# Kernel tuning notes

Hardware: AMD Instinct MI355X
Metric: run time of the kernel (lower is better)

The kernel has to match this reference:

```python
import jax, jax.numpy as jnp
import numpy as np

INNER_LR = 0.01        # inner-loop fast-weight learning rate
ADAPTER_SCALE = 1.0    # adapter_scale from __init__
INIT_STD = 0.001       # init_std for phi_0 fast-weight initialization
VOCAB = 32000


def setup_inputs() -> dict:
    key = jax.random.key(0)
    k1, k2, k3, k4, k5 = jax.random.split(key, 5)
    B, S, H, R, V = 2, 2048, 1024, 16, VOCAB
    hidden_states = jax.random.normal(k1, (B, S, H), dtype=jnp.float32)
    input_ids = jax.random.randint(k2, (B, S), 0, V)
    # phi_0 learned fast-weight initialization (init_std-scaled, per TTTMetaAdapter)
    fast_a = jax.random.normal(k3, (H, R), dtype=jnp.float32) * INIT_STD
    fast_b = jax.random.normal(k4, (R, H), dtype=jnp.float32) * INIT_STD
    lm_head = jax.random.normal(k5, (H, V), dtype=jnp.float32) * 0.02
    return {"hidden_states": hidden_states, "input_ids": input_ids,
            "fast_a": fast_a, "fast_b": fast_b, "lm_head": lm_head}


def _next_token_loss(logits, input_ids):
    # ttt_next_token_loss_from_logits: CE(logits[:, :-1], input_ids[:, 1:])
    logp = jax.nn.log_softmax(logits[:, :-1, :], axis=-1)       # [B, S-1, V]
    tgt = input_ids[:, 1:]                                       # [B, S-1]
    nll = -jnp.take_along_axis(logp, tgt[..., None], axis=-1)[..., 0]
    return nll.mean()


def _apply(hidden_states, a, b):
    # TTTState.apply: h + (h @ fast_a @ fast_b) * scale
    return hidden_states + ((hidden_states @ a) @ b) * ADAPTER_SCALE


def reference(hidden_states, input_ids, fast_a, fast_b, lm_head):
    # Inner objective: next-token CE of adapted hidden states through lm_head.
    def inner_loss(a, b):
        adapted = _apply(hidden_states, a, b)                    # [B, S, H]
        logits = adapted @ lm_head                               # [B, S, V]
        return _next_token_loss(logits, input_ids)

    loss, (ga, gb) = jax.value_and_grad(inner_loss, argnums=(0, 1))(fast_a, fast_b)
    grad_norm = jnp.sqrt(jnp.sum(ga * ga) + jnp.sum(gb * gb))
    # One differentiable TTT inner gradient step on the fast weights.
    new_a = fast_a - INNER_LR * ga
    new_b = fast_b - INNER_LR * gb
    out = _apply(hidden_states, new_a, new_b)                    # adapted output
    return out, new_a, new_b, loss, grad_norm
```

## Files before the change

kernel.cpp:

```cpp
#include <hip/hip_runtime.h>
#include <hip/hip_bf16.h>


#define ROWS 4096
#define Hdim 1024
#define Rdim 16
#define Vdim 32000
#define NVALID 4094.0f
#define LRATE 0.01f
#define RB 32
#define VT 512

typedef __attribute__((ext_vector_type(8))) short bf16x8;
typedef __attribute__((ext_vector_type(4))) float f32x4;

static __device__ __forceinline__ float bf2f(short u) {
  union { float f; unsigned int i; } w; w.i = ((unsigned int)(unsigned short)u) << 16; return w.f;
}
static __device__ __forceinline__ short f2bf(float f) {
  union { float f; unsigned int i; } w; w.f = f;
  unsigned int lsb = (w.i >> 16) & 1u;
  w.i += 0x7fffu + lsb;
  return (short)(w.i >> 16);
}
static __device__ __forceinline__ f32x4 mfma16(bf16x8 a, bf16x8 b, f32x4 c) {
  return __builtin_amdgcn_mfma_f32_16x16x32_bf16(a, b, c, 0, 0, 0);
}

#define OFF_BP2   ((size_t)0)
#define OFF_BP1   ((size_t)65536000)
#define OFF_ADP   ((size_t)131072000)
#define OFF_DA    ((size_t)139460608)
#define OFF_U     ((size_t)156237824)
#define OFF_DU    ((size_t)156499968)
#define OFF_Z     ((size_t)157024256)
#define OFF_GA    ((size_t)157089792)
#define OFF_GB    ((size_t)157155328)
#define OFF_LOSS  ((size_t)157220864)

#define OUT_A    ((size_t)4194304)
#define OUT_B    ((size_t)4210688)
#define OUT_LOSS ((size_t)4227072)
#define OUT_GN   ((size_t)4227073)

__global__ void k_pack(const float* __restrict__ in, short* __restrict__ Bp1,
                       short* __restrict__ Bp2) {
  __shared__ short tile[32][258];
  int v0 = blockIdx.x * 256, k0 = blockIdx.y * 32;
  int tid = threadIdx.x;
#pragma unroll
  for (int r = 0; r < 32; ++r)
    tile[r][tid] = f2bf(in[(size_t)(k0 + r) * Vdim + v0 + tid]);
  __syncthreads();
  int lane = tid & 63, l15 = lane & 15, q = (lane >> 4) & 3, g = tid >> 6;
#pragma unroll
  for (int it = 0; it < 4; ++it) {
    int vbl = it * 4 + g;
    bf16x8 frag;
#pragma unroll
    for (int j = 0; j < 8; ++j) frag[j] = tile[q * 8 + j][vbl * 16 + l15];
    *(bf16x8*)(Bp1 + ((size_t)(v0 / 16 + vbl) * 32 + k0 / 32) * 512 + lane * 8) = frag;
  }
#pragma unroll
  for (int it = 0; it < 4; ++it) {
    int idx = it * 4 + g;
    int hbl = idx >> 3, vkbl = idx & 7;
    bf16x8 frag;
#pragma unroll
    for (int j = 0; j < 8; ++j) frag[j] = tile[hbl * 16 + l15][vkbl * 32 + q * 8 + j];
    *(bf16x8*)(Bp2 + ((size_t)(k0 / 16 + hbl) * 1000 + v0 / 32 + vkbl) * 512 + lane * 8) = frag;
  }
}

__global__ void k_prep_ua(const float* __restrict__ hs, const float* __restrict__ fa,
                          const float* __restrict__ fb, float* __restrict__ u,
                          short* __restrict__ adp) {
  __shared__ float wred[4][16];
  __shared__ float ubc[16];
  int row = blockIdx.x, tid = threadIdx.x, lane = tid & 63, w = tid >> 6;
  const float* hrow = hs + (size_t)row * Hdim;
  float4 hv = *(const float4*)(hrow + tid * 4);
  float ur[16];
  const float* fap = fa + (size_t)tid * 4 * Rdim;
#pragma unroll
  for (int r = 0; r < 16; ++r)
    ur[r] = hv.x * fap[r] + hv.y * fap[16 + r] + hv.z * fap[32 + r] + hv.w * fap[48 + r];
#pragma unroll
  for (int r = 0; r < 16; ++r)
#pragma unroll
    for (int off = 32; off; off >>= 1) ur[r] += __shfl_xor(ur[r], off);
  if (lane == 0) {
#pragma unroll
    for (int r = 0; r < 16; ++r) wred[w][r] = ur[r];
  }
  __syncthreads();
  if (tid < 16) {
    float s = wred[0][tid] + wred[1][tid] + wred[2][tid] + wred[3][tid];
    ubc[tid] = s;
    u[row * Rdim + tid] = s;
  }
  __syncthreads();
  float a0 = hv.x, a1 = hv.y, a2 = hv.z, a3 = hv.w;
#pragma unroll
  for (int r = 0; r < 16; ++r) {
    float uv = ubc[r];
    float4 bv = *(const float4*)(fb + r * Hdim + tid * 4);
    a0 += uv * bv.x; a1 += uv * bv.y; a2 += uv * bv.z; a3 += uv * bv.w;
  }
  short4 o; o.x = f2bf(a0); o.y = f2bf(a1); o.z = f2bf(a2); o.w = f2bf(a3);
  *(short4*)(adp + (size_t)row * Hdim + tid * 4) = o;
}

__launch_bounds__(1024, 4)
__global__ void k_fused(const short* __restrict__ adp, const short* __restrict__ Bp1,
                        const short* __restrict__ Bp2, short* __restrict__ dApart,
                        float* __restrict__ zpart) {
  __shared__ __align__(16) short lA[RB * 1024];
  __shared__ __align__(16) short lP[2][RB * VT];
  __shared__ float zred[RB * 16];
  int tid = threadIdx.x, lane = tid & 63, w = tid >> 6;
  int q = lane >> 4, l15 = lane & 15;
  int L = blockIdx.x;
  int sp = (L >> 2) & 1;
  int rg = (L & 3) | ((L >> 3) << 2);
  int row0 = rg * RB;
  int v0beg = sp ? 15872 : 0;
  int v0end = sp ? 32000 : 15872;
  int nt = sp ? 32 : 31;

#pragma unroll
  for (int i = 0; i < 4; ++i) {
    int idx = tid + i * 1024;
    int r = idx >> 7, c8 = (idx & 127) * 8;
    bf16x8 vv = *(const bf16x8*)(adp + (size_t)(row0 + r) * Hdim + c8);
    *(bf16x8*)((char*)lA + r * 2048 + ((c8 * 2) ^ ((r & 7) << 4))) = vv;
  }
  if (tid < RB * 16) zred[tid] = 0.f;

  float zacc[8];
  f32x4 acc[2][4];
#pragma unroll
  for (int j = 0; j < 8; ++j) zacc[j] = 0.f;
#pragma unroll
  for (int rf = 0; rf < 2; ++rf)
#pragma unroll
    for (int cf = 0; cf < 4; ++cf)
#pragma unroll
      for (int i = 0; i < 4; ++i) acc[rf][cf][i] = 0.f;

  __syncthreads();

  for (int t = 0; t < nt; ++t) {
    int v0 = v0beg + t * VT;
    int rem = v0end - v0; if (rem > VT) rem = VT;
    char* lPc = (char*)lP[t & 1];
    f32x4 lacc[2][2];
#pragma unroll
    for (int rf = 0; rf < 2; ++rf)
#pragma unroll
      for (int cf = 0; cf < 2; ++cf)
#pragma unroll
        for (int i = 0; i < 4; ++i) lacc[rf][cf][i] = 0.f;
#pragma unroll 8
    for (int ks = 0; ks < 32; ++ks) {
      int kgl = ks * 32 + q * 8;
      bf16x8 af[2], bfr[2];
#pragma unroll
      for (int rf = 0; rf < 2; ++rf) {
        int r = rf * 16 + l15;
        af[rf] = *(const bf16x8*)((const char*)lA + r * 2048 + ((kgl * 2) ^ ((r & 7) << 4)));
      }
#pragma unroll
      for (int cf = 0; cf < 2; ++cf) {
        int vb = v0 / 16 + w * 2 + cf;
        if (vb > 1999) vb = 1999;
        bfr[cf] = *(const bf16x8*)(Bp1 + ((size_t)vb * 32 + ks) * 512 + lane * 8);
      }
#pragma unroll
      for (int rf = 0; rf < 2; ++rf)
#pragma unroll
        for (int cf = 0; cf < 2; ++cf)
          lacc[rf][cf] = mfma16(af[rf], bfr[cf], lacc[rf][cf]);
    }
#pragma unroll
    for (int rf = 0; rf < 2; ++rf)
#pragma unroll
      for (int i = 0; i < 4; ++i) {
        int r = rf * 16 + q * 4 + i;
        float z = 0.f;
#pragma unroll
        for (int cf = 0; cf < 2; ++cf) {
          int c0 = w * 32 + cf * 16;
          float pv = (c0 < rem) ? __expf(lacc[rf][cf][i]) : 0.f;
          z += pv;
          int c = c0 + l15;
          *(short*)(lPc + r * 1024 + ((c * 2) ^ ((r & 7) << 4))) = f2bf(pv);
        }
#pragma unroll
        for (int off = 1; off < 16; off <<= 1) z += __shfl_xor(z, off);
        if (l15 == 0) zred[r * 16 + w] += z;
      }
    __syncthreads();
#pragma unroll 4
    for (int ks = 0; ks < 16; ++ks) {
      int kb = ks * 32 + q * 8;
      int vkb = v0 / 32 + ks;
      if (vkb > 999) vkb = 999;
      bf16x8 pa[2], bg[4];
#pragma unroll
      for (int rf = 0; rf < 2; ++rf) {
        int r = rf * 16 + l15;
        pa[rf] = *(const bf16x8*)(lPc + r * 1024 + ((kb * 2) ^ ((r & 7) << 4)));
      }
#pragma unroll
      for (int cf = 0; cf < 4; ++cf)
        bg[cf] = *(const bf16x8*)(Bp2 + ((size_t)(w * 4 + cf) * 1000 + vkb) * 512 + lane * 8);
#pragma unroll
      for (int rf = 0; rf < 2; ++rf)
#pragma unroll
        for (int cf = 0; cf < 4; ++cf)
          acc[rf][cf] = mfma16(pa[rf], bg[cf], acc[rf][cf]);
    }
  }
  __syncthreads();
  if (tid < RB) {
    float z = 0.f;
#pragma unroll
    for (int g = 0; g < 16; ++g) z += zred[tid * 16 + g];
    zpart[sp * ROWS + row0 + tid] = z;
  }
#pragma unroll
  for (int rf = 0; rf < 2; ++rf)
#pragma unroll
    for (int cf = 0; cf < 4; ++cf)
#pragma unroll
      for (int i = 0; i < 4; ++i) {
        int r = rf * 16 + q * 4 + i;
        int h = w * 64 + cf * 16 + l15;
        dApart[((size_t)(row0 + r) * 2 + sp) * Hdim + h] = f2bf(acc[rf][cf][i]);
      }
}

__global__ void k_post_du(const short* __restrict__ adp, const short* __restrict__ Bp1,
                          const float* __restrict__ fb, const int* __restrict__ ids,
                          const float* __restrict__ zpart, char* __restrict__ dAx,
                          float* __restrict__ du, float* __restrict__ loss_acc) {
  __shared__ float red[256];
  __shared__ float wredu[4][16];
  int row = blockIdx.x, tid = threadIdx.x, lane = tid & 63, w = tid >> 6;
  int b = row >> 11, s = row & 2047;
  bool valid = s < 2047;
  float Z = zpart[row] + zpart[ROWS + row];
  float sc = 1.f / (Z * NVALID);
  int tgt = valid ? ids[b * 2048 + s + 1] : 0;
  const short* prow = (const short*)(dAx + (size_t)row * 4096);
  size_t vbb = (size_t)(tgt >> 4) * 32;
  int l15t = tgt & 15;
  short4 p0 = *(const short4*)(prow + tid * 4);
  short4 p1 = *(const short4*)(prow + 1024 + tid * 4);
  short4 a4 = *(const short4*)(adp + (size_t)row * Hdim + tid * 4);
  float lcv[4], d[4];
#pragma unroll
  for (int c = 0; c < 4; ++c) {
    int h = tid * 4 + c;
    short lcs = Bp1[(vbb + (h >> 5)) * 512 + (size_t)((l15t + 16 * ((h >> 3) & 3)) * 8 + (h & 7))];
    lcv[c] = bf2f(lcs);
  }
  float pp0[4] = {bf2f(p0.x), bf2f(p0.y), bf2f(p0.z), bf2f(p0.w)};
  float pp1[4] = {bf2f(p1.x), bf2f(p1.y), bf2f(p1.z), bf2f(p1.w)};
  float avv[4] = {bf2f(a4.x), bf2f(a4.y), bf2f(a4.z), bf2f(a4.w)};
#pragma unroll
  for (int c = 0; c < 4; ++c)
    d[c] = valid ? ((pp0[c] + pp1[c]) * sc - lcv[c] * (1.f / NVALID)) : 0.f;
  __syncthreads();
  float* drow = (float*)(dAx + (size_t)row * 4096);
  float dot = 0.f;
#pragma unroll
  for (int c = 0; c < 4; ++c) {
    drow[tid * 4 + c] = d[c];
    dot += avv[c] * lcv[c];
  }
  float pdu[16];
#pragma unroll
  for (int r = 0; r < 16; ++r) {
    float4 bv = *(const float4*)(fb + r * Hdim + tid * 4);
    pdu[r] = d[0] * bv.x + d[1] * bv.y + d[2] * bv.z + d[3] * bv.w;
  }
#pragma unroll
  for (int r = 0; r < 16; ++r)
#pragma unroll
    for (int off = 32; off; off >>= 1) pdu[r] += __shfl_xor(pdu[r], off);
  if (lane == 0) {
#pragma unroll
    for (int r = 0; r < 16; ++r) wredu[w][r] = pdu[r];
  }
  red[tid] = dot;
  __syncthreads();
  if (tid < 16)
    du[row * Rdim + tid] = wredu[0][tid] + wredu[1][tid] + wredu[2][tid] + wredu[3][tid];
  if (!valid) return;
  for (int o = 128; o; o >>= 1) {
    if (tid < o) red[tid] += red[tid + o];
    __syncthreads();
  }
  if (tid == 0) atomicAdd(loss_acc, (logf(Z) - red[0]) / NVALID);
}

__global__ void k_ga_gb(const float* __restrict__ hs, const float* __restrict__ dA,
                        const float* __restrict__ u, const float* __restrict__ du,
                        float* __restrict__ ga, float* __restrict__ gb) {
  __shared__ float lu[512 * 16], ldu[512 * 16];
  int tid = threadIdx.x;
  int h = blockIdx.x * 256 + tid;
  int r0 = blockIdx.y * 512;
#pragma unroll
  for (int i = 0; i < 32; ++i) {
    int idx = tid + i * 256;
    lu[idx] = u[(size_t)r0 * Rdim + idx];
    ldu[idx] = du[(size_t)r0 * Rdim + idx];
  }
  __syncthreads();
  float aga[16], agb[16];
#pragma unroll
  for (int r = 0; r < 16; ++r) { aga[r] = 0.f; agb[r] = 0.f; }
  for (int rl = 0; rl < 512; ++rl) {
    int row = r0 + rl;
    float hv = hs[(size_t)row * Hdim + h];
    float dv = dA[(size_t)row * Hdim + h];
#pragma unroll
    for (int r = 0; r < 16; ++r) {
      aga[r] += hv * ldu[rl * 16 + r];
      agb[r] += lu[rl * 16 + r] * dv;
    }
  }
#pragma unroll
  for (int r = 0; r < 16; ++r) {
    atomicAdd(&ga[h * Rdim + r], aga[r]);
    atomicAdd(&gb[r * Hdim + h], agb[r]);
  }
}

__global__ void k_finalize(const float* __restrict__ fa, const float* __restrict__ fb,
                           const float* __restrict__ ga, const float* __restrict__ gb,
                           const float* __restrict__ loss_acc, float* __restrict__ out) {
  __shared__ float red[512];
  int tid = threadIdx.x;
  float s = 0.f;
  for (int i = tid; i < 32768; i += 512) {
    float g = ga[i];
    s += g * g;
  }
  red[tid] = s; __syncthreads();
  for (int o = 256; o; o >>= 1) {
    if (tid < o) red[tid] += red[tid + o];
    __syncthreads();
  }
  float gn = sqrtf(red[0]);
  for (int i = tid; i < 16384; i += 512) {
    out[OUT_A + i] = fa[i] - LRATE * ga[i];
    out[OUT_B + i] = fb[i] - LRATE * gb[i];
  }
  if (tid == 0) { out[OUT_LOSS] = loss_acc[0]; out[OUT_GN] = gn; }
}

__global__ void k_tail_uo(const float* __restrict__ hs, const float* __restrict__ outAB,
                          float* __restrict__ out) {
  __shared__ float wred[4][16];
  __shared__ float ubc[16];
  int row = blockIdx.x, tid = threadIdx.x, lane = tid & 63, w = tid >> 6;
  const float* na = outAB;
  const float* nb = outAB + 16384;
  const float* hrow = hs + (size_t)row * Hdim;
  float4 hv = *(const float4*)(hrow + tid * 4);
  float ur[16];
  const float* nap = na + (size_t)tid * 4 * Rdim;
#pragma unroll
  for (int r = 0; r < 16; ++r)
    ur[r] = hv.x * nap[r] + hv.y * nap[16 + r] + hv.z * nap[32 + r] + hv.w * nap[48 + r];
#pragma unroll
  for (int r = 0; r < 16; ++r)
#pragma unroll
    for (int off = 32; off; off >>= 1) ur[r] += __shfl_xor(ur[r], off);
  if (lane == 0) {
#pragma unroll
    for (int r = 0; r < 16; ++r) wred[w][r] = ur[r];
  }
  __syncthreads();
  if (tid < 16) ubc[tid] = wred[0][tid] + wred[1][tid] + wred[2][tid] + wred[3][tid];
  __syncthreads();
  float a0 = hv.x, a1 = hv.y, a2 = hv.z, a3 = hv.w;
#pragma unroll
  for (int r = 0; r < 16; ++r) {
    float uv = ubc[r];
    float4 bv = *(const float4*)(nb + r * Hdim + tid * 4);
    a0 += uv * bv.x; a1 += uv * bv.y; a2 += uv * bv.z; a3 += uv * bv.w;
  }
  float4 o; o.x = a0; o.y = a1; o.z = a2; o.w = a3;
  *(float4*)(out + (size_t)row * Hdim + tid * 4) = o;
}

extern "C" void kernel_launch(void* const* d_in, const int* in_sizes, int n_in,
                              void* d_out, int out_size, void* d_ws, size_t ws_size,
                              hipStream_t stream) {
  (void)in_sizes; (void)n_in; (void)out_size; (void)ws_size;
  const float* hs   = (const float*)d_in[0];
  const int*   ids  = (const int*)d_in[1];
  const float* fa   = (const float*)d_in[2];
  const float* fb   = (const float*)d_in[3];
  const float* lmhf = (const float*)d_in[4];
  float* out = (float*)d_out;
  char* ws = (char*)d_ws;

  short* Bp2    = (short*)(ws + OFF_BP2);
  short* Bp1    = (short*)(ws + OFF_BP1);
  short* adp    = (short*)(ws + OFF_ADP);
  char*  dAx    = ws + OFF_DA;
  float* u      = (float*)(ws + OFF_U);
  float* du     = (float*)(ws + OFF_DU);
  float* zpart  = (float*)(ws + OFF_Z);
  float* ga     = (float*)(ws + OFF_GA);
  float* gb     = (float*)(ws + OFF_GB);
  float* loss_acc = (float*)(ws + OFF_LOSS);

  hipMemsetAsync(ws + OFF_GA, 0, 65536 * 2 + 4, stream);

  k_pack<<<dim3(125, 32), 256, 0, stream>>>(lmhf, Bp1, Bp2);
  k_prep_ua<<<4096, 256, 0, stream>>>(hs, fa, fb, u, adp);
  k_fused<<<256, 1024, 0, stream>>>(adp, Bp1, Bp2, (short*)dAx, zpart);
  k_post_du<<<4096, 256, 0, stream>>>(adp, Bp1, fb, ids, zpart, dAx, du, loss_acc);
  k_ga_gb<<<dim3(4, 8), 256, 0, stream>>>(hs, (float*)dAx, u, du, ga, gb);
  k_finalize<<<1, 512, 0, stream>>>(fa, fb, ga, gb, loss_acc, out);
  k_tail_uo<<<4096, 256, 0, stream>>>(hs, out + OUT_A, out);
}
```

Baseline: 1.085 ms.

## Use FP8 MFMA for logits GEMM and split vocab four ways

The forward logits GEMM (adapted hidden × lm_head) now uses FP8 inputs with the fp8 MFMA instruction, and k_pack and k_prep_ua write FP8 copies of lm_head and the adapted activations. The fused kernel moves to 512-thread blocks with a four-way vocab split, 512 blocks, wider per-wave tiles and a single P buffer. Z partials are accumulated in registers and reduced once at the end. Target logit columns are now read from the bf16 transposed pack. This halves operand bandwidth and doubles MFMA rate for the first GEMM, at the cost of FP8 precision in the logits. The change also adds more partial dA traffic and an extra barrier per tile.

```diff
diff --git a/kernel.cpp b/kernel.cpp
--- a/kernel.cpp
+++ b/kernel.cpp
@@ -10,6 +10,9 @@
 #define LRATE 0.01f
 #define RB 32
 #define VT 512
+#define SPW 8000
+#define LAS 1032
+#define LPS 1040
 
 typedef __attribute__((ext_vector_type(8))) short bf16x8;
 typedef __attribute__((ext_vector_type(4))) float f32x4;
@@ -26,40 +29,52 @@
 static __device__ __forceinline__ f32x4 mfma16(bf16x8 a, bf16x8 b, f32x4 c) {
   return __builtin_amdgcn_mfma_f32_16x16x32_bf16(a, b, c, 0, 0, 0);
 }
+static __device__ __forceinline__ f32x4 mfma8(long a, long b, f32x4 c) {
+  return __builtin_amdgcn_mfma_f32_16x16x32_fp8_fp8(a, b, c, 0, 0, 0);
+}
+static __device__ __forceinline__ int pk4fp8(float f0, float f1, float f2, float f3) {
+  int v = __builtin_amdgcn_cvt_pk_fp8_f32(f0, f1, 0, false);
+  v = __builtin_amdgcn_cvt_pk_fp8_f32(f2, f3, v, true);
+  return v;
+}
 
 #define OFF_BP2   ((size_t)0)
 #define OFF_BP1   ((size_t)65536000)
-#define OFF_ADP   ((size_t)131072000)
-#define OFF_DA    ((size_t)139460608)
-#define OFF_U     ((size_t)156237824)
-#define OFF_DU    ((size_t)156499968)
-#define OFF_Z     ((size_t)157024256)
-#define OFF_GA    ((size_t)157089792)
-#define OFF_GB    ((size_t)157155328)
-#define OFF_LOSS  ((size_t)157220864)
+#define OFF_ADP   ((size_t)98304000)
+#define OFF_ADP8  ((size_t)106692608)
+#define OFF_DAX   ((size_t)110886912)
+#define OFF_U     ((size_t)144441344)
+#define OFF_DU    ((size_t)144703488)
+#define OFF_Z     ((size_t)144965632)
+#define OFF_GA    ((size_t)145031168)
+#define OFF_GB    ((size_t)145096704)
+#define OFF_LOSS  ((size_t)145162240)
 
 #define OUT_A    ((size_t)4194304)
 #define OUT_B    ((size_t)4210688)
 #define OUT_LOSS ((size_t)4227072)
 #define OUT_GN   ((size_t)4227073)
 
-__global__ void k_pack(const float* __restrict__ in, short* __restrict__ Bp1,
+__global__ void k_pack(const float* __restrict__ in, char* __restrict__ Bp1,
                        short* __restrict__ Bp2) {
-  __shared__ short tile[32][258];
+  __shared__ float tile[32][260];
   int v0 = blockIdx.x * 256, k0 = blockIdx.y * 32;
   int tid = threadIdx.x;
 #pragma unroll
   for (int r = 0; r < 32; ++r)
-    tile[r][tid] = f2bf(in[(size_t)(k0 + r) * Vdim + v0 + tid]);
+    tile[r][tid] = in[(size_t)(k0 + r) * Vdim + v0 + tid];
   __syncthreads();
   int lane = tid & 63, l15 = lane & 15, q = (lane >> 4) & 3, g = tid >> 6;
 #pragma unroll
   for (int it = 0; it < 4; ++it) {
     int vbl = it * 4 + g;
-    bf16x8 frag;
-#pragma unroll
-    for (int j = 0; j < 8; ++j) frag[j] = tile[q * 8 + j][vbl * 16 + l15];
-    *(bf16x8*)(Bp1 + ((size_t)(v0 / 16 + vbl) * 32 + k0 / 32) * 512 + lane * 8) = frag;
+    float f[8];
+#pragma unroll
+    for (int j = 0; j < 8; ++j) f[j] = tile[q * 8 + j][vbl * 16 + l15];
+    int2 w2;
+    w2.x = pk4fp8(f[0], f[1], f[2], f[3]);
+    w2.y = pk4fp8(f[4], f[5], f[6], f[7]);
+    *(int2*)(Bp1 + ((size_t)(v0 / 16 + vbl) * 32 + k0 / 32) * 512 + lane * 8) = w2;
   }
 #pragma unroll
   for (int it = 0; it < 4; ++it) {
@@ -67,14 +82,14 @@
     int hbl = idx >> 3, vkbl = idx & 7;
     bf16x8 frag;
 #pragma unroll
-    for (int j = 0; j < 8; ++j) frag[j] = tile[hbl * 16 + l15][vkbl * 32 + q * 8 + j];
+    for (int j = 0; j < 8; ++j) frag[j] = f2bf(tile[hbl * 16 + l15][vkbl * 32 + q * 8 + j]);
     *(bf16x8*)(Bp2 + ((size_t)(k0 / 16 + hbl) * 1000 + v0 / 32 + vkbl) * 512 + lane * 8) = frag;
   }
 }
 
 __global__ void k_prep_ua(const float* __restrict__ hs, const float* __restrict__ fa,
                           const float* __restrict__ fb, float* __restrict__ u,
-                          short* __restrict__ adp) {
+                          short* __restrict__ adp, char* __restrict__ adp8) {
   __shared__ float wred[4][16];
   __shared__ float ubc[16];
   int row = blockIdx.x, tid = threadIdx.x, lane = tid & 63, w = tid >> 6;
@@ -109,139 +124,132 @@
   }
   short4 o; o.x = f2bf(a0); o.y = f2bf(a1); o.z = f2bf(a2); o.w = f2bf(a3);
   *(short4*)(adp + (size_t)row * Hdim + tid * 4) = o;
-}
-
-__launch_bounds__(1024, 4)
-__global__ void k_fused(const short* __restrict__ adp, const short* __restrict__ Bp1,
+  *(int*)(adp8 + (size_t)row * Hdim + tid * 4) = pk4fp8(a0, a1, a2, a3);
+}
+
+__launch_bounds__(512, 4)
+__global__ void k_fused(const char* __restrict__ adp8, const char* __restrict__ Bp1,
                         const short* __restrict__ Bp2, short* __restrict__ dApart,
                         float* __restrict__ zpart) {
-  __shared__ __align__(16) short lA[RB * 1024];
-  __shared__ __align__(16) short lP[2][RB * VT];
-  __shared__ float zred[RB * 16];
+  __shared__ __align__(16) char lA[RB * LAS];
+  __shared__ __align__(16) char lP[RB * LPS];
+  __shared__ float zred[RB * 8];
   int tid = threadIdx.x, lane = tid & 63, w = tid >> 6;
   int q = lane >> 4, l15 = lane & 15;
-  int L = blockIdx.x;
-  int sp = (L >> 2) & 1;
-  int rg = (L & 3) | ((L >> 3) << 2);
+  int sp = blockIdx.x & 3, rg = blockIdx.x >> 2;
   int row0 = rg * RB;
-  int v0beg = sp ? 15872 : 0;
-  int v0end = sp ? 32000 : 15872;
-  int nt = sp ? 32 : 31;
-
-#pragma unroll
-  for (int i = 0; i < 4; ++i) {
-    int idx = tid + i * 1024;
-    int r = idx >> 7, c8 = (idx & 127) * 8;
-    bf16x8 vv = *(const bf16x8*)(adp + (size_t)(row0 + r) * Hdim + c8);
-    *(bf16x8*)((char*)lA + r * 2048 + ((c8 * 2) ^ ((r & 7) << 4))) = vv;
-  }
-  if (tid < RB * 16) zred[tid] = 0.f;
+  int v0beg = sp * SPW;
+
+#pragma unroll
+  for (int i = 0; i < 8; ++i) {
+    int idx = tid + i * 512;
+    int r = idx >> 7, kk8 = (idx & 127) * 8;
+    *(int2*)(lA + r * LAS + kk8) = *(const int2*)(adp8 + (size_t)(row0 + r) * Hdim + kk8);
+  }
 
   float zacc[8];
-  f32x4 acc[2][4];
+  f32x4 acc[2][8];
 #pragma unroll
   for (int j = 0; j < 8; ++j) zacc[j] = 0.f;
 #pragma unroll
   for (int rf = 0; rf < 2; ++rf)
 #pragma unroll
-    for (int cf = 0; cf < 4; ++cf)
+    for (int cf = 0; cf < 8; ++cf)
 #pragma unroll
       for (int i = 0; i < 4; ++i) acc[rf][cf][i] = 0.f;
 
   __syncthreads();
 
-  for (int t = 0; t < nt; ++t) {
+  for (int t = 0; t < 16; ++t) {
     int v0 = v0beg + t * VT;
-    int rem = v0end - v0; if (rem > VT) rem = VT;
-    char* lPc = (char*)lP[t & 1];
-    f32x4 lacc[2][2];
+    int rem = (t == 15) ? 320 : 512;
+    f32x4 lacc[2][4];
 #pragma unroll
     for (int rf = 0; rf < 2; ++rf)
 #pragma unroll
-      for (int cf = 0; cf < 2; ++cf)
+      for (int cf = 0; cf < 4; ++cf)
 #pragma unroll
         for (int i = 0; i < 4; ++i) lacc[rf][cf][i] = 0.f;
 #pragma unroll 8
     for (int ks = 0; ks < 32; ++ks) {
-      int kgl = ks * 32 + q * 8;
-      bf16x8 af[2], bfr[2];
-#pragma unroll
-      for (int rf = 0; rf < 2; ++rf) {
-        int r = rf * 16 + l15;
-        af[rf] = *(const bf16x8*)((const char*)lA + r * 2048 + ((kgl * 2) ^ ((r & 7) << 4)));
+      int kk = ks * 32 + q * 8;
+      long af[2], bfr[4];
+      af[0] = *(const long*)(lA + l15 * LAS + kk);
+      af[1] = *(const long*)(lA + (16 + l15) * LAS + kk);
+#pragma unroll
+      for (int cf = 0; cf < 4; ++cf) {
+        int vb = v0 / 16 + w * 4 + cf;
+        if (vb > 1999) vb = 1999;
+        bfr[cf] = *(const long*)(Bp1 + ((size_t)vb * 32 + ks) * 512 + lane * 8);
       }
 #pragma unroll
-      for (int cf = 0; cf < 2; ++cf) {
-        int vb = v0 / 16 + w * 2 + cf;
-        if (vb > 1999) vb = 1999;
-        bfr[cf] = *(const bf16x8*)(Bp1 + ((size_t)vb * 32 + ks) * 512 + lane * 8);
-      }
-#pragma unroll
       for (int rf = 0; rf < 2; ++rf)
 #pragma unroll
-        for (int cf = 0; cf < 2; ++cf)
-          lacc[rf][cf] = mfma16(af[rf], bfr[cf], lacc[rf][cf]);
+        for (int cf = 0; cf < 4; ++cf)
+          lacc[rf][cf] = mfma8(af[rf], bfr[cf], lacc[rf][cf]);
     }
 #pragma unroll
     for (int rf = 0; rf < 2; ++rf)
 #pragma unroll
       for (int i = 0; i < 4; ++i) {
         int r = rf * 16 + q * 4 + i;
-        float z = 0.f;
-#pragma unroll
-        for (int cf = 0; cf < 2; ++cf) {
-          int c0 = w * 32 + cf * 16;
+#pragma unroll
+        for (int cf = 0; cf < 4; ++cf) {
+          int c0 = w * 64 + cf * 16;
           float pv = (c0 < rem) ? __expf(lacc[rf][cf][i]) : 0.f;
-          z += pv;
-          int c = c0 + l15;
-          *(short*)(lPc + r * 1024 + ((c * 2) ^ ((r & 7) << 4))) = f2bf(pv);
+          zacc[rf * 4 + i] += pv;
+          *(short*)(lP + r * LPS + (c0 + l15) * 2) = f2bf(pv);
         }
-#pragma unroll
-        for (int off = 1; off < 16; off <<= 1) z += __shfl_xor(z, off);
-        if (l15 == 0) zred[r * 16 + w] += z;
       }
     __syncthreads();
 #pragma unroll 4
     for (int ks = 0; ks < 16; ++ks) {
-      int kb = ks * 32 + q * 8;
+      int kb2 = ks * 64 + q * 16;
       int vkb = v0 / 32 + ks;
       if (vkb > 999) vkb = 999;
-      bf16x8 pa[2], bg[4];
-#pragma unroll
-      for (int rf = 0; rf < 2; ++rf) {
-        int r = rf * 16 + l15;
-        pa[rf] = *(const bf16x8*)(lPc + r * 1024 + ((kb * 2) ^ ((r & 7) << 4)));
-      }
-#pragma unroll
-      for (int cf = 0; cf < 4; ++cf)
-        bg[cf] = *(const bf16x8*)(Bp2 + ((size_t)(w * 4 + cf) * 1000 + vkb) * 512 + lane * 8);
+      bf16x8 pa[2], bg[8];
+      pa[0] = *(const bf16x8*)(lP + l15 * LPS + kb2);
+      pa[1] = *(const bf16x8*)(lP + (16 + l15) * LPS + kb2);
+#pragma unroll
+      for (int cf = 0; cf < 8; ++cf)
+        bg[cf] = *(const bf16x8*)(Bp2 + ((size_t)(w * 8 + cf) * 1000 + vkb) * 512 + lane * 8);
 #pragma unroll
       for (int rf = 0; rf < 2; ++rf)
 #pragma unroll
-        for (int cf = 0; cf < 4; ++cf)
+        for (int cf = 0; cf < 8; ++cf)
           acc[rf][cf] = mfma16(pa[rf], bg[cf], acc[rf][cf]);
     }
-  }
+    __syncthreads();
+  }
+#pragma unroll
+  for (int rf = 0; rf < 2; ++rf)
+#pragma unroll
+    for (int i = 0; i < 4; ++i) {
+      float z = zacc[rf * 4 + i];
+#pragma unroll
+      for (int off = 1; off < 16; off <<= 1) z += __shfl_xor(z, off);
+      if (l15 == 0) zred[(rf * 16 + q * 4 + i) * 8 + w] = z;
+    }
   __syncthreads();
   if (tid < RB) {
     float z = 0.f;
 #pragma unroll
-    for (int g = 0; g < 16; ++g) z += zred[tid * 16 + g];
+    for (int g = 0; g < 8; ++g) z += zred[tid * 8 + g];
     zpart[sp * ROWS + row0 + tid] = z;
   }
 #pragma unroll
   for (int rf = 0; rf < 2; ++rf)
 #pragma unroll
-    for (int cf = 0; cf < 4; ++cf)
+    for (int cf = 0; cf < 8; ++cf)
 #pragma unroll
       for (int i = 0; i < 4; ++i) {
         int r = rf * 16 + q * 4 + i;
-        int h = w * 64 + cf * 16 + l15;
-        dApart[((size_t)(row0 + r) * 2 + sp) * Hdim + h] = f2bf(acc[rf][cf][i]);
+        int h = w * 128 + cf * 16 + l15;
+        dApart[((size_t)(row0 + r) * 4 + sp) * Hdim + h] = f2bf(acc[rf][cf][i]);
       }
 }
 
-__global__ void k_post_du(const short* __restrict__ adp, const short* __restrict__ Bp1,
+__global__ void k_post_du(const short* __restrict__ adp, const short* __restrict__ Bp2,
                           const float* __restrict__ fb, const int* __restrict__ ids,
                           const float* __restrict__ zpart, char* __restrict__ dAx,
                           float* __restrict__ du, float* __restrict__ loss_acc) {
@@ -250,30 +258,34 @@
   int row = blockIdx.x, tid = threadIdx.x, lane = tid & 63, w = tid >> 6;
   int b = row >> 11, s = row & 2047;
   bool valid = s < 2047;
-  float Z = zpart[row] + zpart[ROWS + row];
+  float Z = zpart[row] + zpart[ROWS + row] + zpart[2 * ROWS + row] + zpart[3 * ROWS + row];
   float sc = 1.f / (Z * NVALID);
   int tgt = valid ? ids[b * 2048 + s + 1] : 0;
-  const short* prow = (const short*)(dAx + (size_t)row * 4096);
-  size_t vbb = (size_t)(tgt >> 4) * 32;
-  int l15t = tgt & 15;
+  const short* prow = (const short*)(dAx + (size_t)row * 8192);
   short4 p0 = *(const short4*)(prow + tid * 4);
   short4 p1 = *(const short4*)(prow + 1024 + tid * 4);
+  short4 p2 = *(const short4*)(prow + 2048 + tid * 4);
+  short4 p3 = *(const short4*)(prow + 3072 + tid * 4);
   short4 a4 = *(const short4*)(adp + (size_t)row * Hdim + tid * 4);
+  int tq = (tgt >> 3) & 3, tj = tgt & 7, tvkb = tgt >> 5;
   float lcv[4], d[4];
 #pragma unroll
   for (int c = 0; c < 4; ++c) {
     int h = tid * 4 + c;
-    short lcs = Bp1[(vbb + (h >> 5)) * 512 + (size_t)((l15t + 16 * ((h >> 3) & 3)) * 8 + (h & 7))];
+    short lcs = Bp2[((size_t)(h >> 4) * 1000 + tvkb) * 512 +
+                    (size_t)(((h & 15) + 16 * tq) * 8 + tj)];
     lcv[c] = bf2f(lcs);
   }
-  float pp0[4] = {bf2f(p0.x), bf2f(p0.y), bf2f(p0.z), bf2f(p0.w)};
-  float pp1[4] = {bf2f(p1.x), bf2f(p1.y), bf2f(p1.z), bf2f(p1.w)};
+  float q0[4] = {bf2f(p0.x), bf2f(p0.y), bf2f(p0.z), bf2f(p0.w)};
+  float q1[4] = {bf2f(p1.x), bf2f(p1.y), bf2f(p1.z), bf2f(p1.w)};
+  float q2[4] = {bf2f(p2.x), bf2f(p2.y), bf2f(p2.z), bf2f(p2.w)};
+  float q3[4] = {bf2f(p3.x), bf2f(p3.y), bf2f(p3.z), bf2f(p3.w)};
   float avv[4] = {bf2f(a4.x), bf2f(a4.y), bf2f(a4.z), bf2f(a4.w)};
 #pragma unroll
   for (int c = 0; c < 4; ++c)
-    d[c] = valid ? ((pp0[c] + pp1[c]) * sc - lcv[c] * (1.f / NVALID)) : 0.f;
-  __syncthreads();
-  float* drow = (float*)(dAx + (size_t)row * 4096);
+    d[c] = valid ? ((q0[c] + q1[c] + q2[c] + q3[c]) * sc - lcv[c] * (1.f / NVALID)) : 0.f;
+  __syncthreads();
+  float* drow = (float*)(dAx + (size_t)row * 8192);
   float dot = 0.f;
 #pragma unroll
   for (int c = 0; c < 4; ++c) {
@@ -326,7 +338,7 @@
   for (int rl = 0; rl < 512; ++rl) {
     int row = r0 + rl;
     float hv = hs[(size_t)row * Hdim + h];
-    float dv = dA[(size_t)row * Hdim + h];
+    float dv = dA[(size_t)row * 2048 + h];
 #pragma unroll
     for (int r = 0; r < 16; ++r) {
       aga[r] += hv * ldu[rl * 16 + r];
@@ -412,9 +424,10 @@
   char* ws = (char*)d_ws;
 
   short* Bp2    = (short*)(ws + OFF_BP2);
-  short* Bp1    = (short*)(ws + OFF_BP1);
+  char*  Bp1    = ws + OFF_BP1;
   short* adp    = (short*)(ws + OFF_ADP);
-  char*  dAx    = ws + OFF_DA;
+  char*  adp8   = ws + OFF_ADP8;
+  char*  dAx    = ws + OFF_DAX;
   float* u      = (float*)(ws + OFF_U);
   float* du     = (float*)(ws + OFF_DU);
   float* zpart  = (float*)(ws + OFF_Z);
@@ -425,9 +438,9 @@
   hipMemsetAsync(ws + OFF_GA, 0, 65536 * 2 + 4, stream);
 
   k_pack<<<dim3(125, 32), 256, 0, stream>>>(lmhf, Bp1, Bp2);
-  k_prep_ua<<<4096, 256, 0, stream>>>(hs, fa, fb, u, adp);
-  k_fused<<<256, 1024, 0, stream>>>(adp, Bp1, Bp2, (short*)dAx, zpart);
-  k_post_du<<<4096, 256, 0, stream>>>(adp, Bp1, fb, ids, zpart, dAx, du, loss_acc);
+  k_prep_ua<<<4096, 256, 0, stream>>>(hs, fa, fb, u, adp, adp8);
+  k_fused<<<512, 512, 0, stream>>>(adp8, Bp1, Bp2, (short*)dAx, zpart);
+  k_post_du<<<4096, 256, 0, stream>>>(adp, Bp2, fb, ids, zpart, dAx, du, loss_acc);
   k_ga_gb<<<dim3(4, 8), 256, 0, stream>>>(hs, (float*)dAx, u, du, ga, gb);
   k_finalize<<<1, 512, 0, stream>>>(fa, fb, ga, gb, loss_acc, out);
   k_tail_uo<<<4096, 256, 0, stream>>>(hs, out + OUT_A, out);
```

Measured after the change: 1.497 ms. 1.38x slower.
